# Optimization experiments

Measured on AMD Instinct MI355X. Metric: run time of the kernel, lower is better.

The kernel has to match this reference:

```python
import jax, jax.numpy as jnp
import numpy as np

B, T, D, F, E, K = 4, 2048, 1024, 2048, 8, 2


def setup_inputs() -> dict:
    key = jax.random.key(0)
    ks = jax.random.split(key, 5)
    s = lambda n: 1.0 / np.sqrt(n)
    return {
        "x": jax.random.normal(ks[0], (B, T, D), jnp.float32),
        "gate_w": jax.random.normal(ks[1], (D, E), jnp.float32) * s(D),
        "gate_b": jnp.zeros((E,), jnp.float32),
        "w1": jax.random.normal(ks[2], (E, D, F), jnp.float32) * s(D),
        "b1": jnp.zeros((E, F), jnp.float32),
        "w2": jax.random.normal(ks[3], (E, F, D), jnp.float32) * s(F),
        "b2": jnp.zeros((E, D), jnp.float32),
    }


def reference(x, gate_w, gate_b, w1, b1, w2, b2):
    # Router: gate logits -> top-k -> softmax over the k selected logits
    logits = x @ gate_w + gate_b                      # [B,T,E]
    top_v, top_i = jax.lax.top_k(logits, K)           # [B,T,K]
    top_w = jax.nn.softmax(top_v, axis=-1)            # [B,T,K]
    # Dense combine weights per expert: w_full[b,t,e] = sum_k top_w * 1[top_i==e]
    one_hot = jax.nn.one_hot(top_i, E, dtype=x.dtype)  # [B,T,K,E]
    w_full = jnp.sum(top_w[..., None] * one_hot, axis=-2)  # [B,T,E]
    # All-experts FFN (batched over expert dim), exact-erf GELU as in nn.GELU()
    h = jax.nn.gelu(jnp.einsum('btd,edf->ebtf', x, w1) + b1[:, None, None, :],
                    approximate=False)                 # [E,B,T,F]
    y = jnp.einsum('ebtf,efd->ebtd', h, w2) + b2[:, None, None, :]  # [E,B,T,D]
    # Weighted combine (zero weight for unselected experts == masked dispatch)
    return jnp.einsum('bte,ebtd->btd', w_full, y)      # [B,T,D]
```

## Files before the change

kernel.cpp:

```cpp
#include <hip/hip_runtime.h>
#include <hip/hip_bf16.h>
#include <math.h>

#define B_ 4
#define T_ 2048
#define D_ 1024
#define F_ 2048
#define E_ 8
#define NT (B_ * T_)
#define NS (NT * 2)
#define CAP (NS + E_ * 128)

typedef __attribute__((ext_vector_type(8))) short short8;
typedef __attribute__((ext_vector_type(4))) float floatx4;

static __device__ __forceinline__ unsigned short f2bf(float f) {
  union { float f; unsigned u; } a; a.f = f;
  unsigned r = a.u + 0x7fffu + ((a.u >> 16) & 1u);
  return (unsigned short)(r >> 16);
}

static __device__ __forceinline__ void gld16(const unsigned short* g, unsigned short* l) {
  __builtin_amdgcn_global_load_lds(
      (const __attribute__((address_space(1))) void*)g,
      (__attribute__((address_space(3))) void*)l, 16, 0, 0);
}

__global__ void transpose_cvt(const float* __restrict__ in, unsigned short* __restrict__ out,
                              int R, int C) {
  __shared__ float tile[32][33];
  int e = blockIdx.z;
  const float* inp = in + (size_t)e * R * C;
  unsigned short* outp = out + (size_t)e * R * C;
  int c0 = blockIdx.x * 32, r0 = blockIdx.y * 32;
  int tx = threadIdx.x, ty = threadIdx.y;
#pragma unroll
  for (int j = 0; j < 4; j++)
    tile[ty + 8 * j][tx] = inp[(size_t)(r0 + ty + 8 * j) * C + c0 + tx];
  __syncthreads();
#pragma unroll
  for (int j = 0; j < 4; j++)
    outp[(size_t)(c0 + ty + 8 * j) * R + r0 + tx] = f2bf(tile[tx][ty + 8 * j]);
}

__global__ void router_k(const float* __restrict__ x, const float* __restrict__ gw,
                         const float* __restrict__ gb, int* __restrict__ ti,
                         float* __restrict__ tw) {
  int wid = threadIdx.x >> 6, lane = threadIdx.x & 63;
  int t = blockIdx.x * 4 + wid;
  const float* xr = x + (size_t)t * D_;
  float acc[E_];
#pragma unroll
  for (int e = 0; e < E_; e++) acc[e] = 0.f;
#pragma unroll
  for (int it = 0; it < D_ / 64; it++) {
    int d = it * 64 + lane;
    float xv = xr[d];
    const float* g = gw + d * E_;
#pragma unroll
    for (int e = 0; e < E_; e++) acc[e] += xv * g[e];
  }
#pragma unroll
  for (int off = 32; off > 0; off >>= 1)
#pragma unroll
    for (int e = 0; e < E_; e++) acc[e] += __shfl_xor(acc[e], off);
  if (lane == 0) {
    float v[E_];
#pragma unroll
    for (int e = 0; e < E_; e++) v[e] = acc[e] + gb[e];
    int i0 = 0; float v0 = v[0];
#pragma unroll
    for (int e = 1; e < E_; e++) if (v[e] > v0) { v0 = v[e]; i0 = e; }
    int i1 = -1; float v1 = -3.4e38f;
#pragma unroll
    for (int e = 0; e < E_; e++) if (e != i0 && v[e] > v1) { v1 = v[e]; i1 = e; }
    float ex = expf(v1 - v0);
    float w0 = 1.f / (1.f + ex);
    float w1 = ex / (1.f + ex);
    ti[2 * t] = i0; tw[2 * t] = w0;
    ti[2 * t + 1] = i1; tw[2 * t + 1] = w1;
  }
}

__global__ void count_prefix_k(const int* __restrict__ ti, int* __restrict__ offs,
                               int* __restrict__ cursors) {
  __shared__ int scnt[4][E_];
  int tid = threadIdx.x;
  int cnt[E_];
#pragma unroll
  for (int k = 0; k < E_; k++) cnt[k] = 0;
  for (int i = tid; i < NS; i += 256) {
    int e = ti[i];
#pragma unroll
    for (int k = 0; k < E_; k++) cnt[k] += (e == k) ? 1 : 0;
  }
#pragma unroll
  for (int off = 32; off > 0; off >>= 1)
#pragma unroll
    for (int k = 0; k < E_; k++) cnt[k] += __shfl_xor(cnt[k], off);
  int wid = tid >> 6, lane = tid & 63;
  if (lane == 0)
#pragma unroll
    for (int k = 0; k < E_; k++) scnt[wid][k] = cnt[k];
  __syncthreads();
  if (tid == 0) {
    int o = 0;
    for (int k = 0; k < E_; k++) {
      int c = scnt[0][k] + scnt[1][k] + scnt[2][k] + scnt[3][k];
      offs[k] = o;
      cursors[k] = o;
      o += (c + 127) & ~127;
    }
    offs[E_] = o;
  }
}

__global__ void fill_k(int* __restrict__ idx, float* __restrict__ wgt) {
  int s = blockIdx.x * 256 + threadIdx.x;
  if (s < CAP) { idx[s] = 0; wgt[s] = 0.f; }
}

__global__ void scatter_k(const int* __restrict__ ti, const float* __restrict__ tw,
                          int* __restrict__ cursors, int* __restrict__ idx,
                          float* __restrict__ wgt) {
  int a = blockIdx.x * 256 + threadIdx.x;
  int lane = threadIdx.x & 63;
  int e = ti[a];
  unsigned long long m[E_];
#pragma unroll
  for (int k = 0; k < E_; k++) m[k] = __ballot(e == k);
  int base = 0;
  if (lane < E_) base = atomicAdd(&cursors[lane], __popcll(m[lane]));
  int myBase = __shfl(base, e);
  unsigned long long m_mine = 0;
#pragma unroll
  for (int k = 0; k < E_; k++) if (e == k) m_mine = m[k];
  int rank = __popcll(m_mine & ((1ull << lane) - 1ull));
  int pos = myBase + rank;
  idx[pos] = a >> 1;
  wgt[pos] = tw[a];
}

__global__ void gather_k(const float* __restrict__ x, const int* __restrict__ idx,
                         unsigned short* __restrict__ Xg) {
  int s = blockIdx.x;
  int t = idx[s];
  const float4* xr = (const float4*)(x + (size_t)t * D_);
  float4 v = xr[threadIdx.x];
  uint2 p;
  p.x = (unsigned)f2bf(v.x) | ((unsigned)f2bf(v.y) << 16);
  p.y = (unsigned)f2bf(v.z) | ((unsigned)f2bf(v.w) << 16);
  ((uint2*)(Xg + (size_t)s * D_))[threadIdx.x] = p;
}

__global__ __launch_bounds__(256) void gemm1_k(const unsigned short* __restrict__ Xg,
                                               const unsigned short* __restrict__ w1t,
                                               const float* __restrict__ b1,
                                               unsigned short* __restrict__ H,
                                               const int* __restrict__ offs) {
  int slot0 = blockIdx.y * 128;
  if (slot0 >= offs[E_]) return;
  int e = 0;
  while (slot0 >= offs[e + 1]) e++;
  const int K = D_;
  const unsigned short* Bp = w1t + (size_t)e * F_ * D_;
  int n0 = blockIdx.x * 128;

  __shared__ unsigned short lA[128 * 32];
  __shared__ unsigned short lB[128 * 32];

  int tid = threadIdx.x;
  int wid = tid >> 6, lane = tid & 63;
  int wr = wid >> 1, wc = wid & 1;
  int quad = lane >> 4, l15 = lane & 15;

  int srow = 32 * wid + (lane >> 2);
  int scol = (lane & 3) * 8;
  const unsigned short* gA0 = Xg + (size_t)(slot0 + srow) * K + scol;
  const unsigned short* gA1 = gA0 + (size_t)16 * K;
  const unsigned short* gB0 = Bp + (size_t)(n0 + srow) * K + scol;
  const unsigned short* gB1 = gB0 + (size_t)16 * K;
  unsigned short* lA0 = &lA[(32 * wid) * 32];
  unsigned short* lA1 = &lA[(32 * wid + 16) * 32];
  unsigned short* lB0 = &lB[(32 * wid) * 32];
  unsigned short* lB1 = &lB[(32 * wid + 16) * 32];

  floatx4 acc[4][4];
#pragma unroll
  for (int mi = 0; mi < 4; mi++)
#pragma unroll
    for (int ni = 0; ni < 4; ni++) acc[mi][ni] = (floatx4){0.f, 0.f, 0.f, 0.f};

  for (int k0 = 0; k0 < K; k0 += 32) {
    gld16(gA0 + k0, lA0);
    gld16(gA1 + k0, lA1);
    gld16(gB0 + k0, lB0);
    gld16(gB1 + k0, lB1);
    __syncthreads();
    short8 af[4], bfr[4];
#pragma unroll
    for (int mi = 0; mi < 4; mi++)
      af[mi] = *(const short8*)&lA[(64 * wr + 16 * mi + l15) * 32 + quad * 8];
#pragma unroll
    for (int ni = 0; ni < 4; ni++)
      bfr[ni] = *(const short8*)&lB[(64 * wc + 16 * ni + l15) * 32 + quad * 8];
#pragma unroll
    for (int mi = 0; mi < 4; mi++)
#pragma unroll
      for (int ni = 0; ni < 4; ni++)
        acc[mi][ni] = __builtin_amdgcn_mfma_f32_16x16x32_bf16(af[mi], bfr[ni], acc[mi][ni], 0, 0, 0);
    __syncthreads();
  }

  const float* bias = b1 + (size_t)e * F_;
#pragma unroll
  for (int mi = 0; mi < 4; mi++) {
    int row = slot0 + 64 * wr + 16 * mi + quad * 4;
#pragma unroll
    for (int ni = 0; ni < 4; ni++) {
      int col = n0 + 64 * wc + 16 * ni + l15;
      float bv = bias[col];
#pragma unroll
      for (int r = 0; r < 4; r++) {
        float v = acc[mi][ni][r] + bv;
        v = 0.5f * v * (1.f + erff(v * 0.70710678118654752f));
        H[(size_t)(row + r) * F_ + col] = f2bf(v);
      }
    }
  }
}

__global__ __launch_bounds__(256) void gemm2_k(const unsigned short* __restrict__ H,
                                               const unsigned short* __restrict__ w2t,
                                               const float* __restrict__ b2,
                                               const int* __restrict__ idx,
                                               const float* __restrict__ wgt,
                                               float* __restrict__ out,
                                               const int* __restrict__ offs) {
  int slot0 = blockIdx.y * 128;
  if (slot0 >= offs[E_]) return;
  int e = 0;
  while (slot0 >= offs[e + 1]) e++;
  const int K = F_;
  const unsigned short* Bp = w2t + (size_t)e * D_ * F_;
  int n0 = blockIdx.x * 128;

  __shared__ unsigned short lA[128 * 32];
  __shared__ unsigned short lB[128 * 32];

  int tid = threadIdx.x;
  int wid = tid >> 6, lane = tid & 63;
  int wr = wid >> 1, wc = wid & 1;
  int quad = lane >> 4, l15 = lane & 15;

  int srow = 32 * wid + (lane >> 2);
  int scol = (lane & 3) * 8;
  const unsigned short* gA0 = H + (size_t)(slot0 + srow) * K + scol;
  const unsigned short* gA1 = gA0 + (size_t)16 * K;
  const unsigned short* gB0 = Bp + (size_t)(n0 + srow) * K + scol;
  const unsigned short* gB1 = gB0 + (size_t)16 * K;
  unsigned short* lA0 = &lA[(32 * wid) * 32];
  unsigned short* lA1 = &lA[(32 * wid + 16) * 32];
  unsigned short* lB0 = &lB[(32 * wid) * 32];
  unsigned short* lB1 = &lB[(32 * wid + 16) * 32];

  floatx4 acc[4][4];
#pragma unroll
  for (int mi = 0; mi < 4; mi++)
#pragma unroll
    for (int ni = 0; ni < 4; ni++) acc[mi][ni] = (floatx4){0.f, 0.f, 0.f, 0.f};

  for (int k0 = 0; k0 < K; k0 += 32) {
    gld16(gA0 + k0, lA0);
    gld16(gA1 + k0, lA1);
    gld16(gB0 + k0, lB0);
    gld16(gB1 + k0, lB1);
    __syncthreads();
    short8 af[4], bfr[4];
#pragma unroll
    for (int mi = 0; mi < 4; mi++)
      af[mi] = *(const short8*)&lA[(64 * wr + 16 * mi + l15) * 32 + quad * 8];
#pragma unroll
    for (int ni = 0; ni < 4; ni++)
      bfr[ni] = *(const short8*)&lB[(64 * wc + 16 * ni + l15) * 32 + quad * 8];
#pragma unroll
    for (int mi = 0; mi < 4; mi++)
#pragma unroll
      for (int ni = 0; ni < 4; ni++)
        acc[mi][ni] = __builtin_amdgcn_mfma_f32_16x16x32_bf16(af[mi], bfr[ni], acc[mi][ni], 0, 0, 0);
    __syncthreads();
  }

  const float* bias = b2 + (size_t)e * D_;
#pragma unroll
  for (int mi = 0; mi < 4; mi++) {
    int row = slot0 + 64 * wr + 16 * mi + quad * 4;
#pragma unroll
    for (int r = 0; r < 4; r++) {
      int slot = row + r;
      int t = idx[slot];
      float w = wgt[slot];
      if (w != 0.f) {
        float* orow = out + (size_t)t * D_;
#pragma unroll
        for (int ni = 0; ni < 4; ni++) {
          int col = n0 + 64 * wc + 16 * ni + l15;
          float v = acc[mi][ni][r] + bias[col];
          atomicAdd(&orow[col], w * v);
        }
      }
    }
  }
}

extern "C" void kernel_launch(void* const* d_in, const int* in_sizes, int n_in,
                              void* d_out, int out_size, void* d_ws, size_t ws_size,
                              hipStream_t stream) {
  const float* x  = (const float*)d_in[0];
  const float* gw = (const float*)d_in[1];
  const float* gb = (const float*)d_in[2];
  const float* w1 = (const float*)d_in[3];
  const float* b1 = (const float*)d_in[4];
  const float* w2 = (const float*)d_in[5];
  const float* b2 = (const float*)d_in[6];
  float* out = (float*)d_out;

  char* p = (char*)d_ws;
  unsigned short* w1t = (unsigned short*)p; p += (size_t)E_ * D_ * F_ * 2;
  unsigned short* w2t = (unsigned short*)p; p += (size_t)E_ * D_ * F_ * 2;
  unsigned short* Xg  = (unsigned short*)p; p += (size_t)CAP * D_ * 2;
  unsigned short* H   = (unsigned short*)p; p += (size_t)CAP * F_ * 2;
  int*   idx = (int*)p;   p += (size_t)CAP * 4;
  float* wgt = (float*)p; p += (size_t)CAP * 4;
  int*   ti  = (int*)p;   p += (size_t)NS * 4;
  float* tw  = (float*)p; p += (size_t)NS * 4;
  int* cursors = (int*)p; p += 64;
  int* offs    = (int*)p; p += 64;

  hipMemsetAsync(out, 0, (size_t)NT * D_ * 4, stream);

  dim3 tb(32, 8);
  transpose_cvt<<<dim3(F_ / 32, D_ / 32, E_), tb, 0, stream>>>(w1, w1t, D_, F_);
  transpose_cvt<<<dim3(D_ / 32, F_ / 32, E_), tb, 0, stream>>>(w2, w2t, F_, D_);
  router_k<<<NT / 4, 256, 0, stream>>>(x, gw, gb, ti, tw);
  count_prefix_k<<<1, 256, 0, stream>>>(ti, offs, cursors);
  fill_k<<<(CAP + 255) / 256, 256, 0, stream>>>(idx, wgt);
  scatter_k<<<NS / 256, 256, 0, stream>>>(ti, tw, cursors, idx, wgt);
  gather_k<<<CAP, 256, 0, stream>>>(x, idx, Xg);
  gemm1_k<<<dim3(F_ / 128, CAP / 128), 256, 0, stream>>>(Xg, w1t, b1, H, offs);
  gemm2_k<<<dim3(D_ / 128, CAP / 128), 256, 0, stream>>>(H, w2t, b2, idx, wgt, out, offs);
}
```

Measured before the change: 558.6 us.

## Swizzle GEMM LDS layout and replace atomic scatter with deterministic combine kernel

Applies an XOR swizzle to the LDS tile column chunks in both expert GEMMs to reduce bank conflicts on the MFMA fragment reads. Gemm2 now writes bf16 per-slot outputs into a buffer that reuses the Xg region, instead of doing fp32 atomic adds into the output. A new combine kernel reads each token's two slot rows, using positions recorded during scatter, and computes the weighted sum. This removes the output memset and the atomics, at the cost of an extra kernel and an extra bf16 round trip of the expert outputs, which adds rounding error.

Result: faster. 479.1 us (-14.2%).

```diff
diff --git a/kernel.cpp b/kernel.cpp
--- a/kernel.cpp
+++ b/kernel.cpp
@@ -18,6 +18,10 @@
   union { float f; unsigned u; } a; a.f = f;
   unsigned r = a.u + 0x7fffu + ((a.u >> 16) & 1u);
   return (unsigned short)(r >> 16);
+}
+
+static __device__ __forceinline__ float bf2f(unsigned u) {
+  union { unsigned u; float f; } a; a.u = u << 16; return a.f;
 }
 
 static __device__ __forceinline__ void gld16(const unsigned short* g, unsigned short* l) {
@@ -115,14 +119,14 @@
   }
 }
 
-__global__ void fill_k(int* __restrict__ idx, float* __restrict__ wgt) {
+__global__ void fill_k(int* __restrict__ idx) {
   int s = blockIdx.x * 256 + threadIdx.x;
-  if (s < CAP) { idx[s] = 0; wgt[s] = 0.f; }
+  if (s < CAP) idx[s] = 0;
 }
 
 __global__ void scatter_k(const int* __restrict__ ti, const float* __restrict__ tw,
                           int* __restrict__ cursors, int* __restrict__ idx,
-                          float* __restrict__ wgt) {
+                          int* __restrict__ pos_of) {
   int a = blockIdx.x * 256 + threadIdx.x;
   int lane = threadIdx.x & 63;
   int e = ti[a];
@@ -138,7 +142,7 @@
   int rank = __popcll(m_mine & ((1ull << lane) - 1ull));
   int pos = myBase + rank;
   idx[pos] = a >> 1;
-  wgt[pos] = tw[a];
+  pos_of[a] = pos;
 }
 
 __global__ void gather_k(const float* __restrict__ x, const int* __restrict__ idx,
@@ -152,6 +156,7 @@
   p.y = (unsigned)f2bf(v.z) | ((unsigned)f2bf(v.w) << 16);
   ((uint2*)(Xg + (size_t)s * D_))[threadIdx.x] = p;
 }
+
 
 __global__ __launch_bounds__(256) void gemm1_k(const unsigned short* __restrict__ Xg,
                                                const unsigned short* __restrict__ w1t,
@@ -173,9 +178,10 @@
   int wid = tid >> 6, lane = tid & 63;
   int wr = wid >> 1, wc = wid & 1;
   int quad = lane >> 4, l15 = lane & 15;
+  int sw = (l15 >> 1) & 3;
 
   int srow = 32 * wid + (lane >> 2);
-  int scol = (lane & 3) * 8;
+  int scol = (((lane & 3) ^ ((lane >> 3) & 3))) * 8;
   const unsigned short* gA0 = Xg + (size_t)(slot0 + srow) * K + scol;
   const unsigned short* gA1 = gA0 + (size_t)16 * K;
   const unsigned short* gB0 = Bp + (size_t)(n0 + srow) * K + scol;
@@ -200,10 +206,10 @@
     short8 af[4], bfr[4];
 #pragma unroll
     for (int mi = 0; mi < 4; mi++)
-      af[mi] = *(const short8*)&lA[(64 * wr + 16 * mi + l15) * 32 + quad * 8];
+      af[mi] = *(const short8*)&lA[(64 * wr + 16 * mi + l15) * 32 + (quad ^ sw) * 8];
 #pragma unroll
     for (int ni = 0; ni < 4; ni++)
-      bfr[ni] = *(const short8*)&lB[(64 * wc + 16 * ni + l15) * 32 + quad * 8];
+      bfr[ni] = *(const short8*)&lB[(64 * wc + 16 * ni + l15) * 32 + (quad ^ sw) * 8];
 #pragma unroll
     for (int mi = 0; mi < 4; mi++)
 #pragma unroll
@@ -233,9 +239,7 @@
 __global__ __launch_bounds__(256) void gemm2_k(const unsigned short* __restrict__ H,
                                                const unsigned short* __restrict__ w2t,
                                                const float* __restrict__ b2,
-                                               const int* __restrict__ idx,
-                                               const float* __restrict__ wgt,
-                                               float* __restrict__ out,
+                                               unsigned short* __restrict__ Yg,
                                                const int* __restrict__ offs) {
   int slot0 = blockIdx.y * 128;
   if (slot0 >= offs[E_]) return;
@@ -252,9 +256,10 @@
   int wid = tid >> 6, lane = tid & 63;
   int wr = wid >> 1, wc = wid & 1;
   int quad = lane >> 4, l15 = lane & 15;
+  int sw = (l15 >> 1) & 3;
 
   int srow = 32 * wid + (lane >> 2);
-  int scol = (lane & 3) * 8;
+  int scol = (((lane & 3) ^ ((lane >> 3) & 3))) * 8;
   const unsigned short* gA0 = H + (size_t)(slot0 + srow) * K + scol;
   const unsigned short* gA1 = gA0 + (size_t)16 * K;
   const unsigned short* gB0 = Bp + (size_t)(n0 + srow) * K + scol;
@@ -279,10 +284,10 @@
     short8 af[4], bfr[4];
 #pragma unroll
     for (int mi = 0; mi < 4; mi++)
-      af[mi] = *(const short8*)&lA[(64 * wr + 16 * mi + l15) * 32 + quad * 8];
+      af[mi] = *(const short8*)&lA[(64 * wr + 16 * mi + l15) * 32 + (quad ^ sw) * 8];
 #pragma unroll
     for (int ni = 0; ni < 4; ni++)
-      bfr[ni] = *(const short8*)&lB[(64 * wc + 16 * ni + l15) * 32 + quad * 8];
+      bfr[ni] = *(const short8*)&lB[(64 * wc + 16 * ni + l15) * 32 + (quad ^ sw) * 8];
 #pragma unroll
     for (int mi = 0; mi < 4; mi++)
 #pragma unroll
@@ -296,21 +301,32 @@
   for (int mi = 0; mi < 4; mi++) {
     int row = slot0 + 64 * wr + 16 * mi + quad * 4;
 #pragma unroll
-    for (int r = 0; r < 4; r++) {
-      int slot = row + r;
-      int t = idx[slot];
-      float w = wgt[slot];
-      if (w != 0.f) {
-        float* orow = out + (size_t)t * D_;
-#pragma unroll
-        for (int ni = 0; ni < 4; ni++) {
-          int col = n0 + 64 * wc + 16 * ni + l15;
-          float v = acc[mi][ni][r] + bias[col];
-          atomicAdd(&orow[col], w * v);
-        }
+    for (int ni = 0; ni < 4; ni++) {
+      int col = n0 + 64 * wc + 16 * ni + l15;
+      float bv = bias[col];
+#pragma unroll
+      for (int r = 0; r < 4; r++) {
+        float v = acc[mi][ni][r] + bv;
+        Yg[(size_t)(row + r) * D_ + col] = f2bf(v);
       }
     }
   }
+}
+
+__global__ void combine_k(const unsigned short* __restrict__ Yg,
+                          const int* __restrict__ pos_of,
+                          const float* __restrict__ tw, float* __restrict__ out) {
+  int t = blockIdx.x;
+  int p0 = pos_of[2 * t], p1 = pos_of[2 * t + 1];
+  float w0 = tw[2 * t], w1 = tw[2 * t + 1];
+  uint2 a = ((const uint2*)(Yg + (size_t)p0 * D_))[threadIdx.x];
+  uint2 b = ((const uint2*)(Yg + (size_t)p1 * D_))[threadIdx.x];
+  float4 r;
+  r.x = w0 * bf2f(a.x & 0xffffu) + w1 * bf2f(b.x & 0xffffu);
+  r.y = w0 * bf2f(a.x >> 16)     + w1 * bf2f(b.x >> 16);
+  r.z = w0 * bf2f(a.y & 0xffffu) + w1 * bf2f(b.y & 0xffffu);
+  r.w = w0 * bf2f(a.y >> 16)     + w1 * bf2f(b.y >> 16);
+  ((float4*)(out + (size_t)t * D_))[threadIdx.x] = r;
 }
 
 extern "C" void kernel_launch(void* const* d_in, const int* in_sizes, int n_in,
@@ -330,23 +346,23 @@
   unsigned short* w2t = (unsigned short*)p; p += (size_t)E_ * D_ * F_ * 2;
   unsigned short* Xg  = (unsigned short*)p; p += (size_t)CAP * D_ * 2;
   unsigned short* H   = (unsigned short*)p; p += (size_t)CAP * F_ * 2;
-  int*   idx = (int*)p;   p += (size_t)CAP * 4;
-  float* wgt = (float*)p; p += (size_t)CAP * 4;
-  int*   ti  = (int*)p;   p += (size_t)NS * 4;
-  float* tw  = (float*)p; p += (size_t)NS * 4;
+  int*   idx    = (int*)p; p += (size_t)CAP * 4;
+  int*   pos_of = (int*)p; p += (size_t)NS * 4;
+  int*   ti     = (int*)p; p += (size_t)NS * 4;
+  float* tw     = (float*)p; p += (size_t)NS * 4;
   int* cursors = (int*)p; p += 64;
   int* offs    = (int*)p; p += 64;
-
-  hipMemsetAsync(out, 0, (size_t)NT * D_ * 4, stream);
+  unsigned short* Yg = Xg;
 
   dim3 tb(32, 8);
   transpose_cvt<<<dim3(F_ / 32, D_ / 32, E_), tb, 0, stream>>>(w1, w1t, D_, F_);
   transpose_cvt<<<dim3(D_ / 32, F_ / 32, E_), tb, 0, stream>>>(w2, w2t, F_, D_);
   router_k<<<NT / 4, 256, 0, stream>>>(x, gw, gb, ti, tw);
   count_prefix_k<<<1, 256, 0, stream>>>(ti, offs, cursors);
-  fill_k<<<(CAP + 255) / 256, 256, 0, stream>>>(idx, wgt);
-  scatter_k<<<NS / 256, 256, 0, stream>>>(ti, tw, cursors, idx, wgt);
+  fill_k<<<(CAP + 255) / 256, 256, 0, stream>>>(idx);
+  scatter_k<<<NS / 256, 256, 0, stream>>>(ti, tw, cursors, idx, pos_of);
   gather_k<<<CAP, 256, 0, stream>>>(x, idx, Xg);
   gemm1_k<<<dim3(F_ / 128, CAP / 128), 256, 0, stream>>>(Xg, w1t, b1, H, offs);
-  gemm2_k<<<dim3(D_ / 128, CAP / 128), 256, 0, stream>>>(H, w2t, b2, idx, wgt, out, offs);
-}
+  gemm2_k<<<dim3(D_ / 128, CAP / 128), 256, 0, stream>>>(H, w2t, b2, Yg, offs);
+  combine_k<<<NT, 256, 0, stream>>>(Yg, pos_of, tw, out);
+}
```
